# Kernel optimization log

Measured on AMD Instinct MI355X. Metric: run time of the kernel, lower is better.

Reference implementation:

```python
import jax, jax.numpy as jnp
import numpy as np

N_NODES = 50000
N_EDGES = 800000
NUM_FEAT = 96
DIM = 64


def _mean_aggregate(x, src, tgt, num_nodes):
    # gather source-node features along edges, sum into targets, divide by in-degree
    msgs = x[src]  # [E, F] irregular gather
    summed = jax.ops.segment_sum(msgs, tgt, num_segments=num_nodes)  # [N, F]
    cnt = jax.ops.segment_sum(jnp.ones((src.shape[0],), x.dtype), tgt, num_segments=num_nodes)
    return summed / jnp.maximum(cnt, 1.0)[:, None]


def _sage_conv(x, src, tgt, W_l, W_r, b):
    # PyG SAGEConv: lin_l(mean_{j in N(i)} x_j) + lin_r(x_i) + bias
    aggr = _mean_aggregate(x, src, tgt, x.shape[0])
    return aggr @ W_l + x @ W_r + b


def setup_inputs() -> dict:
    key = jax.random.key(0)
    ks = jax.random.split(key, 8)
    x = jax.random.normal(ks[0], (N_NODES, NUM_FEAT), dtype=jnp.float32)
    edge_index = jax.random.randint(ks[1], (2, N_EDGES), 0, N_NODES, dtype=jnp.int32)
    s = 0.05
    Wl1 = jax.random.normal(ks[2], (NUM_FEAT, DIM), dtype=jnp.float32) * s
    Wr1 = jax.random.normal(ks[3], (NUM_FEAT, DIM), dtype=jnp.float32) * s
    b1 = jnp.zeros((DIM,), dtype=jnp.float32)
    Wl2 = jax.random.normal(ks[4], (DIM, DIM), dtype=jnp.float32) * s
    Wr2 = jax.random.normal(ks[5], (DIM, DIM), dtype=jnp.float32) * s
    b2 = jnp.zeros((DIM,), dtype=jnp.float32)
    return {"x": x, "edge_index": edge_index, "Wl1": Wl1, "Wr1": Wr1, "b1": b1,
            "Wl2": Wl2, "Wr2": Wr2, "b2": b2}


def reference(x, edge_index, Wl1, Wr1, b1, Wl2, Wr2, b2):
    src, tgt = edge_index[0], edge_index[1]
    h = jax.nn.relu(_sage_conv(x, src, tgt, Wl1, Wr1, b1))
    # F.dropout(..., training=self.training): evaluated in eval mode -> identity
    out = _sage_conv(h, src, tgt, Wl2, Wr2, b2)
    return out
```

## Files before the change

### kernel.cpp

```cpp
#include <hip/hip_runtime.h>
#include <hip/hip_bf16.h>

#define NFEAT 96
#define DIM 64


__global__ void k_hist(const int* __restrict__ tgt, int* __restrict__ cnt, int E,
                       int part_size) {
    const int part = blockIdx.x & 7;
    const int q = blockIdx.x >> 3;
    const int nq = gridDim.x >> 3;
    const int stride = nq * blockDim.x;
    for (int i = q * blockDim.x + threadIdx.x; i < E; i += stride) {
        const int tg = tgt[i];
        if (tg / part_size == part) atomicAdd(&cnt[tg], 1);
    }
}


__global__ void k_scan1(const int* __restrict__ cnt, int* __restrict__ bsum, int N) {
    __shared__ int ws[4];
    const int t = threadIdx.x;
    const int lane = t & 63, w = t >> 6;
    const int base = blockIdx.x * 1024 + t * 4;
    int s = 0;
    if (base + 3 < N) {
        int4 v = *reinterpret_cast<const int4*>(cnt + base);
        s = v.x + v.y + v.z + v.w;
    } else {
        for (int i = 0; i < 4; ++i)
            if (base + i < N) s += cnt[base + i];
    }
    for (int off = 32; off; off >>= 1) s += __shfl_down(s, off, 64);
    if (lane == 0) ws[w] = s;
    __syncthreads();
    if (t == 0) bsum[blockIdx.x] = ws[0] + ws[1] + ws[2] + ws[3];
}

__global__ void k_scan2(const int* __restrict__ bsum, int* __restrict__ boff,
                        int* __restrict__ rowstart, int nb, int N) {
    const int lane = threadIdx.x;
    int carry = 0;
    for (int b0 = 0; b0 < nb; b0 += 64) {
        int i = b0 + lane;
        int orig = (i < nb) ? bsum[i] : 0;
        int v = orig;
        for (int off = 1; off < 64; off <<= 1) {
            int u = __shfl_up(v, off, 64);
            if (lane >= off) v += u;
        }
        if (i < nb) boff[i] = carry + v - orig;
        carry += __shfl(v, 63, 64);
    }
    if (lane == 0) rowstart[N] = carry;
}

__global__ void k_scan3(const int* __restrict__ cnt, const int* __restrict__ boff,
                        int* __restrict__ rowstart, int* __restrict__ wpos, int N) {
    __shared__ int wsum[4];
    const int t = threadIdx.x;
    const int lane = t & 63, w = t >> 6;
    const int base = blockIdx.x * 1024 + t * 4;
    int4 v = make_int4(0, 0, 0, 0);
    if (base + 3 < N) {
        v = *reinterpret_cast<const int4*>(cnt + base);
    } else {
        int* p = &v.x;
        for (int i = 0; i < 4; ++i)
            if (base + i < N) p[i] = cnt[base + i];
    }
    const int s = v.x + v.y + v.z + v.w;
    int inc = s;
    for (int off = 1; off < 64; off <<= 1) {
        int u = __shfl_up(inc, off, 64);
        if (lane >= off) inc += u;
    }
    if (lane == 63) wsum[w] = inc;
    __syncthreads();
    int woff = 0;
    for (int i = 0; i < w; ++i) woff += wsum[i];
    int r = boff[blockIdx.x] + woff + inc - s;
    if (base + 0 < N) { rowstart[base + 0] = r; wpos[base + 0] = r; } r += v.x;
    if (base + 1 < N) { rowstart[base + 1] = r; wpos[base + 1] = r; } r += v.y;
    if (base + 2 < N) { rowstart[base + 2] = r; wpos[base + 2] = r; } r += v.z;
    if (base + 3 < N) { rowstart[base + 3] = r; wpos[base + 3] = r; }
}

__global__ void k_scatter(const int* __restrict__ src, const int* __restrict__ tgt,
                          int* __restrict__ wpos, int* __restrict__ csr_src, int E,
                          int part_size) {
    const int part = blockIdx.x & 7;
    const int q = blockIdx.x >> 3;
    const int nq = gridDim.x >> 3;
    const int stride = nq * blockDim.x;
    for (int i = q * blockDim.x + threadIdx.x; i < E; i += stride) {
        const int tg = tgt[i];
        if (tg / part_size == part) {
            const int p = atomicAdd(&wpos[tg], 1);
            csr_src[p] = src[i];
        }
    }
}

template <int K>
__global__ __launch_bounds__(256) void k_mm(const float* __restrict__ X,
                                            const float* __restrict__ Wl,
                                            const float* __restrict__ Wr,
                                            const float* __restrict__ b,
                                            __hip_bfloat16* __restrict__ A,
                                            float* __restrict__ B, int N) {
    constexpr int ROWS = 32;
    __shared__ float xs[ROWS * K];
    const int t = threadIdx.x;
    const int lane = t & 63;
    const int w = t >> 6;
    const int r0 = blockIdx.x * ROWS;
    const int nvalid = min(ROWS, N - r0);

    {
        const float4* src = reinterpret_cast<const float4*>(X + (size_t)r0 * K);
        float4* dst = reinterpret_cast<float4*>(xs);
        const int nv4 = (nvalid * K) >> 2;
        for (int c = t; c < nv4; c += 256) dst[c] = src[c];
    }
    const float bias = b[lane];
    __syncthreads();

    const int rw = w * 8;
    float accl[8], accr[8];
#pragma unroll
    for (int i = 0; i < 8; ++i) { accl[i] = 0.f; accr[i] = 0.f; }

    for (int k = 0; k < K; k += 4) {
        const float wl0 = Wl[(k + 0) * DIM + lane];
        const float wl1 = Wl[(k + 1) * DIM + lane];
        const float wl2 = Wl[(k + 2) * DIM + lane];
        const float wl3 = Wl[(k + 3) * DIM + lane];
        const float wr0 = Wr[(k + 0) * DIM + lane];
        const float wr1 = Wr[(k + 1) * DIM + lane];
        const float wr2 = Wr[(k + 2) * DIM + lane];
        const float wr3 = Wr[(k + 3) * DIM + lane];
#pragma unroll
        for (int i = 0; i < 8; ++i) {
            const float4 xv = *reinterpret_cast<const float4*>(&xs[(rw + i) * K + k]);
            accl[i] = fmaf(xv.x, wl0, accl[i]);
            accl[i] = fmaf(xv.y, wl1, accl[i]);
            accl[i] = fmaf(xv.z, wl2, accl[i]);
            accl[i] = fmaf(xv.w, wl3, accl[i]);
            accr[i] = fmaf(xv.x, wr0, accr[i]);
            accr[i] = fmaf(xv.y, wr1, accr[i]);
            accr[i] = fmaf(xv.z, wr2, accr[i]);
            accr[i] = fmaf(xv.w, wr3, accr[i]);
        }
    }
#pragma unroll
    for (int i = 0; i < 8; ++i) {
        const int r = r0 + rw + i;
        if (r < N) {
            A[(size_t)r * DIM + lane] = __float2bfloat16(accl[i]);
            B[(size_t)r * DIM + lane] = accr[i] + bias;
        }
    }
}

template <bool RELU>
__global__ void k_aggr(const __hip_bfloat16* __restrict__ A, const float* __restrict__ Bm,
                       const int* __restrict__ rowstart, const int* __restrict__ csr_src,
                       float* __restrict__ out, int N) {
    const int lane = threadIdx.x & 63;
    const int wave = blockIdx.x * (blockDim.x >> 6) + (threadIdx.x >> 6);
    const int nwaves = gridDim.x * (blockDim.x >> 6);
    for (int n = wave; n < N; n += nwaves) {
        const int r0 = rowstart[n];
        const int r1 = rowstart[n + 1];
        float s0 = 0.f, s1 = 0.f, s2 = 0.f, s3 = 0.f;
        int j = r0;
        for (; j + 3 < r1; j += 4) {
            const int c0 = csr_src[j];
            const int c1 = csr_src[j + 1];
            const int c2 = csr_src[j + 2];
            const int c3 = csr_src[j + 3];
            s0 += __bfloat162float(A[(size_t)c0 * DIM + lane]);
            s1 += __bfloat162float(A[(size_t)c1 * DIM + lane]);
            s2 += __bfloat162float(A[(size_t)c2 * DIM + lane]);
            s3 += __bfloat162float(A[(size_t)c3 * DIM + lane]);
        }
        for (; j < r1; ++j) s0 += __bfloat162float(A[(size_t)csr_src[j] * DIM + lane]);
        const float c = (float)(r1 - r0);
        float v = ((s0 + s1) + (s2 + s3)) / fmaxf(c, 1.f) + Bm[(size_t)n * DIM + lane];
        if (RELU) v = fmaxf(v, 0.f);
        out[(size_t)n * DIM + lane] = v;
    }
}

extern "C" void kernel_launch(void* const* d_in, const int* in_sizes, int n_in,
                              void* d_out, int out_size, void* d_ws, size_t ws_size,
                              hipStream_t stream) {
    const float* x   = (const float*)d_in[0];
    const int*   ei  = (const int*)d_in[1];
    const float* Wl1 = (const float*)d_in[2];
    const float* Wr1 = (const float*)d_in[3];
    const float* b1  = (const float*)d_in[4];
    const float* Wl2 = (const float*)d_in[5];
    const float* Wr2 = (const float*)d_in[6];
    const float* b2  = (const float*)d_in[7];
    float* out = (float*)d_out;

    const int N = in_sizes[0] / NFEAT;
    const int E = in_sizes[1] / 2;
    const int* src = ei;
    const int* tgt = ei + E;

    char* ws = (char*)d_ws;
    size_t off = 0;
    auto alloc = [&](size_t bytes) -> void* {
        void* p = ws + off;
        off = (off + bytes + 255) & ~(size_t)255;
        return p;
    };
    const int nb = (N + 1023) / 1024;
    int*   cnt      = (int*)alloc((size_t)N * 4);
    int*   rowstart = (int*)alloc((size_t)(N + 1) * 4);
    int*   wpos     = (int*)alloc((size_t)N * 4);
    int*   bsum     = (int*)alloc((size_t)nb * 4);
    int*   boff     = (int*)alloc((size_t)nb * 4);
    int*   csr      = (int*)alloc((size_t)E * 4);
    __hip_bfloat16* A = (__hip_bfloat16*)alloc((size_t)N * DIM * 2);
    float* B        = (float*)alloc((size_t)N * DIM * 4);
    float* H        = (float*)alloc((size_t)N * DIM * 4);

    hipMemsetAsync(cnt, 0, (size_t)N * 4, stream);

    const int part_size = (N + 7) / 8;
    k_hist<<<2048, 256, 0, stream>>>(tgt, cnt, E, part_size);
    k_scan1<<<nb, 256, 0, stream>>>(cnt, bsum, N);
    k_scan2<<<1, 64, 0, stream>>>(bsum, boff, rowstart, nb, N);
    k_scan3<<<nb, 256, 0, stream>>>(cnt, boff, rowstart, wpos, N);
    k_scatter<<<2048, 256, 0, stream>>>(src, tgt, wpos, csr, E, part_size);

    const int mm_blocks = (N + 31) / 32;

    k_mm<NFEAT><<<mm_blocks, 256, 0, stream>>>(x, Wl1, Wr1, b1, A, B, N);
    k_aggr<true><<<2048, 256, 0, stream>>>(A, B, rowstart, csr, H, N);

    k_mm<DIM><<<mm_blocks, 256, 0, stream>>>(H, Wl2, Wr2, b2, A, B, N);
    k_aggr<false><<<2048, 256, 0, stream>>>(A, B, rowstart, csr, out, N);
}
```

Before: 273.2 us.

## Fuse first-layer matmul with degree histogram and store root term in bf16

Result: faster. 264.8 us (-3.1%).

```diff
diff --git a/kernel.cpp b/kernel.cpp
--- a/kernel.cpp
+++ b/kernel.cpp
@@ -4,16 +4,143 @@
 #define NFEAT 96
 #define DIM 64
 
-
-__global__ void k_hist(const int* __restrict__ tgt, int* __restrict__ cnt, int E,
-                       int part_size) {
-    const int part = blockIdx.x & 7;
-    const int q = blockIdx.x >> 3;
-    const int nq = gridDim.x >> 3;
-    const int stride = nq * blockDim.x;
-    for (int i = q * blockDim.x + threadIdx.x; i < E; i += stride) {
-        const int tg = tgt[i];
-        if (tg / part_size == part) atomicAdd(&cnt[tg], 1);
+template <int K>
+__global__ __launch_bounds__(256) void k_mm_hist(const float* __restrict__ X,
+                                                 const float* __restrict__ Wl,
+                                                 const float* __restrict__ Wr,
+                                                 const float* __restrict__ b,
+                                                 __hip_bfloat16* __restrict__ A,
+                                                 __hip_bfloat16* __restrict__ B, int N,
+                                                 const int* __restrict__ tgt,
+                                                 int* __restrict__ cnt, int E,
+                                                 int part_size, int mmB) {
+    constexpr int ROWS = 32;
+    __shared__ float xs[ROWS * K];
+    const int t = threadIdx.x;
+
+    if ((int)blockIdx.x >= mmB) {
+        const int part = blockIdx.x & 7;
+        const int hb = blockIdx.x - mmB;
+        const int q = hb >> 3;
+        const int nq = (gridDim.x - mmB) >> 3;
+        const int stride = nq * blockDim.x;
+        for (int i = q * blockDim.x + t; i < E; i += stride) {
+            const int tg = tgt[i];
+            if (tg / part_size == part) atomicAdd(&cnt[tg], 1);
+        }
+        return;
+    }
+
+    const int lane = t & 63;
+    const int w = t >> 6;
+    const int r0 = blockIdx.x * ROWS;
+    const int nvalid = min(ROWS, N - r0);
+
+    if (nvalid > 0) {
+        const float4* src = reinterpret_cast<const float4*>(X + (size_t)r0 * K);
+        float4* dst = reinterpret_cast<float4*>(xs);
+        const int nv4 = (nvalid * K) >> 2;
+        for (int c = t; c < nv4; c += 256) dst[c] = src[c];
+    }
+    const float bias = b[lane];
+    __syncthreads();
+    if (nvalid <= 0) return;
+
+    const int rw = w * 8;
+    float accl[8], accr[8];
+#pragma unroll
+    for (int i = 0; i < 8; ++i) { accl[i] = 0.f; accr[i] = 0.f; }
+
+    for (int k = 0; k < K; k += 4) {
+        const float wl0 = Wl[(k + 0) * DIM + lane];
+        const float wl1 = Wl[(k + 1) * DIM + lane];
+        const float wl2 = Wl[(k + 2) * DIM + lane];
+        const float wl3 = Wl[(k + 3) * DIM + lane];
+        const float wr0 = Wr[(k + 0) * DIM + lane];
+        const float wr1 = Wr[(k + 1) * DIM + lane];
+        const float wr2 = Wr[(k + 2) * DIM + lane];
+        const float wr3 = Wr[(k + 3) * DIM + lane];
+#pragma unroll
+        for (int i = 0; i < 8; ++i) {
+            const float4 xv = *reinterpret_cast<const float4*>(&xs[(rw + i) * K + k]);
+            accl[i] = fmaf(xv.x, wl0, accl[i]);
+            accl[i] = fmaf(xv.y, wl1, accl[i]);
+            accl[i] = fmaf(xv.z, wl2, accl[i]);
+            accl[i] = fmaf(xv.w, wl3, accl[i]);
+            accr[i] = fmaf(xv.x, wr0, accr[i]);
+            accr[i] = fmaf(xv.y, wr1, accr[i]);
+            accr[i] = fmaf(xv.z, wr2, accr[i]);
+            accr[i] = fmaf(xv.w, wr3, accr[i]);
+        }
+    }
+#pragma unroll
+    for (int i = 0; i < 8; ++i) {
+        const int r = r0 + rw + i;
+        if (r < N) {
+            A[(size_t)r * DIM + lane] = __float2bfloat16(accl[i]);
+            B[(size_t)r * DIM + lane] = __float2bfloat16(accr[i] + bias);
+        }
+    }
+}
+
+template <int K>
+__global__ __launch_bounds__(256) void k_mm(const float* __restrict__ X,
+                                            const float* __restrict__ Wl,
+                                            const float* __restrict__ Wr,
+                                            const float* __restrict__ b,
+                                            __hip_bfloat16* __restrict__ A,
+                                            __hip_bfloat16* __restrict__ B, int N) {
+    constexpr int ROWS = 32;
+    __shared__ float xs[ROWS * K];
+    const int t = threadIdx.x;
+    const int lane = t & 63;
+    const int w = t >> 6;
+    const int r0 = blockIdx.x * ROWS;
+    const int nvalid = min(ROWS, N - r0);
+
+    {
+        const float4* src = reinterpret_cast<const float4*>(X + (size_t)r0 * K);
+        float4* dst = reinterpret_cast<float4*>(xs);
+        const int nv4 = (nvalid * K) >> 2;
+        for (int c = t; c < nv4; c += 256) dst[c] = src[c];
+    }
+    const float bias = b[lane];
+    __syncthreads();
+
+    const int rw = w * 8;
+    float accl[8], accr[8];
+#pragma unroll
+    for (int i = 0; i < 8; ++i) { accl[i] = 0.f; accr[i] = 0.f; }
+
+    for (int k = 0; k < K; k += 4) {
+        const float wl0 = Wl[(k + 0) * DIM + lane];
+        const float wl1 = Wl[(k + 1) * DIM + lane];
+        const float wl2 = Wl[(k + 2) * DIM + lane];
+        const float wl3 = Wl[(k + 3) * DIM + lane];
+        const float wr0 = Wr[(k + 0) * DIM + lane];
+        const float wr1 = Wr[(k + 1) * DIM + lane];
+        const float wr2 = Wr[(k + 2) * DIM + lane];
+        const float wr3 = Wr[(k + 3) * DIM + lane];
+#pragma unroll
+        for (int i = 0; i < 8; ++i) {
+            const float4 xv = *reinterpret_cast<const float4*>(&xs[(rw + i) * K + k]);
+            accl[i] = fmaf(xv.x, wl0, accl[i]);
+            accl[i] = fmaf(xv.y, wl1, accl[i]);
+            accl[i] = fmaf(xv.z, wl2, accl[i]);
+            accl[i] = fmaf(xv.w, wl3, accl[i]);
+            accr[i] = fmaf(xv.x, wr0, accr[i]);
+            accr[i] = fmaf(xv.y, wr1, accr[i]);
+            accr[i] = fmaf(xv.z, wr2, accr[i]);
+            accr[i] = fmaf(xv.w, wr3, accr[i]);
+        }
+    }
+#pragma unroll
+    for (int i = 0; i < 8; ++i) {
+        const int r = r0 + rw + i;
+        if (r < N) {
+            A[(size_t)r * DIM + lane] = __float2bfloat16(accl[i]);
+            B[(size_t)r * DIM + lane] = __float2bfloat16(accr[i] + bias);
+        }
     }
 }
 
@@ -102,69 +229,9 @@
     }
 }
 
-template <int K>
-__global__ __launch_bounds__(256) void k_mm(const float* __restrict__ X,
-                                            const float* __restrict__ Wl,
-                                            const float* __restrict__ Wr,
-                                            const float* __restrict__ b,
-                                            __hip_bfloat16* __restrict__ A,
-                                            float* __restrict__ B, int N) {
-    constexpr int ROWS = 32;
-    __shared__ float xs[ROWS * K];
-    const int t = threadIdx.x;
-    const int lane = t & 63;
-    const int w = t >> 6;
-    const int r0 = blockIdx.x * ROWS;
-    const int nvalid = min(ROWS, N - r0);
-
-    {
-        const float4* src = reinterpret_cast<const float4*>(X + (size_t)r0 * K);
-        float4* dst = reinterpret_cast<float4*>(xs);
-        const int nv4 = (nvalid * K) >> 2;
-        for (int c = t; c < nv4; c += 256) dst[c] = src[c];
-    }
-    const float bias = b[lane];
-    __syncthreads();
-
-    const int rw = w * 8;
-    float accl[8], accr[8];
-#pragma unroll
-    for (int i = 0; i < 8; ++i) { accl[i] = 0.f; accr[i] = 0.f; }
-
-    for (int k = 0; k < K; k += 4) {
-        const float wl0 = Wl[(k + 0) * DIM + lane];
-        const float wl1 = Wl[(k + 1) * DIM + lane];
-        const float wl2 = Wl[(k + 2) * DIM + lane];
-        const float wl3 = Wl[(k + 3) * DIM + lane];
-        const float wr0 = Wr[(k + 0) * DIM + lane];
-        const float wr1 = Wr[(k + 1) * DIM + lane];
-        const float wr2 = Wr[(k + 2) * DIM + lane];
-        const float wr3 = Wr[(k + 3) * DIM + lane];
-#pragma unroll
-        for (int i = 0; i < 8; ++i) {
-            const float4 xv = *reinterpret_cast<const float4*>(&xs[(rw + i) * K + k]);
-            accl[i] = fmaf(xv.x, wl0, accl[i]);
-            accl[i] = fmaf(xv.y, wl1, accl[i]);
-            accl[i] = fmaf(xv.z, wl2, accl[i]);
-            accl[i] = fmaf(xv.w, wl3, accl[i]);
-            accr[i] = fmaf(xv.x, wr0, accr[i]);
-            accr[i] = fmaf(xv.y, wr1, accr[i]);
-            accr[i] = fmaf(xv.z, wr2, accr[i]);
-            accr[i] = fmaf(xv.w, wr3, accr[i]);
-        }
-    }
-#pragma unroll
-    for (int i = 0; i < 8; ++i) {
-        const int r = r0 + rw + i;
-        if (r < N) {
-            A[(size_t)r * DIM + lane] = __float2bfloat16(accl[i]);
-            B[(size_t)r * DIM + lane] = accr[i] + bias;
-        }
-    }
-}
-
 template <bool RELU>
-__global__ void k_aggr(const __hip_bfloat16* __restrict__ A, const float* __restrict__ Bm,
+__global__ void k_aggr(const __hip_bfloat16* __restrict__ A,
+                       const __hip_bfloat16* __restrict__ Bm,
                        const int* __restrict__ rowstart, const int* __restrict__ csr_src,
                        float* __restrict__ out, int N) {
     const int lane = threadIdx.x & 63;
@@ -187,7 +254,8 @@
         }
         for (; j < r1; ++j) s0 += __bfloat162float(A[(size_t)csr_src[j] * DIM + lane]);
         const float c = (float)(r1 - r0);
-        float v = ((s0 + s1) + (s2 + s3)) / fmaxf(c, 1.f) + Bm[(size_t)n * DIM + lane];
+        float v = ((s0 + s1) + (s2 + s3)) / fmaxf(c, 1.f) +
+                  __bfloat162float(Bm[(size_t)n * DIM + lane]);
         if (RELU) v = fmaxf(v, 0.f);
         out[(size_t)n * DIM + lane] = v;
     }
@@ -226,21 +294,23 @@
     int*   boff     = (int*)alloc((size_t)nb * 4);
     int*   csr      = (int*)alloc((size_t)E * 4);
     __hip_bfloat16* A = (__hip_bfloat16*)alloc((size_t)N * DIM * 2);
-    float* B        = (float*)alloc((size_t)N * DIM * 4);
+    __hip_bfloat16* B = (__hip_bfloat16*)alloc((size_t)N * DIM * 2);
     float* H        = (float*)alloc((size_t)N * DIM * 4);
 
     hipMemsetAsync(cnt, 0, (size_t)N * 4, stream);
 
     const int part_size = (N + 7) / 8;
-    k_hist<<<2048, 256, 0, stream>>>(tgt, cnt, E, part_size);
+    const int mm_blocks = (N + 31) / 32;
+    const int mmB = (mm_blocks + 7) & ~7;
+    const int histB = 2048;
+
+    k_mm_hist<NFEAT><<<mmB + histB, 256, 0, stream>>>(x, Wl1, Wr1, b1, A, B, N,
+                                                      tgt, cnt, E, part_size, mmB);
     k_scan1<<<nb, 256, 0, stream>>>(cnt, bsum, N);
     k_scan2<<<1, 64, 0, stream>>>(bsum, boff, rowstart, nb, N);
     k_scan3<<<nb, 256, 0, stream>>>(cnt, boff, rowstart, wpos, N);
     k_scatter<<<2048, 256, 0, stream>>>(src, tgt, wpos, csr, E, part_size);
 
-    const int mm_blocks = (N + 31) / 32;
-
-    k_mm<NFEAT><<<mm_blocks, 256, 0, stream>>>(x, Wl1, Wr1, b1, A, B, N);
     k_aggr<true><<<2048, 256, 0, stream>>>(A, B, rowstart, csr, H, N);
 
     k_mm<DIM><<<mm_blocks, 256, 0, stream>>>(H, Wl2, Wr2, b2, A, B, N);
```
